# Kernel optimization log

Hardware: AMD Instinct MI355X
Metric: run time of the kernel (lower is better)

The kernel has to match this reference:

```python
import jax, jax.numpy as jnp
import numpy as np

NUM_LEVELS = 16
LEVEL_DIM = 2
BASE_RES = 16
LOG2_HASH = 24
DESIRED_RES = 2048
D = 2
PRIMES = (1, 2654435761)
N_POINTS = 2097152
HIDDEN = 64
OUT_DIM = 3
LC_INIT = 1e-4


def _level_meta():
    # torch-ngp gridencoder level geometry (align_corners=False)
    S = np.log2(DESIRED_RES / BASE_RES) / (NUM_LEVELS - 1)
    max_params = 2 ** LOG2_HASH
    scales, res, offsets = [], [], [0]
    for l in range(NUM_LEVELS):
        s = 2.0 ** (l * S) * BASE_RES - 1.0
        r = int(np.ceil(s)) + 1
        p = min(max_params, (r + 1) ** D)
        p = int(np.ceil(p / 8) * 8)  # align to 8
        scales.append(s)
        res.append(r)
        offsets.append(offsets[-1] + p)
    return scales, res, offsets

SCALES, RES, OFFSETS = _level_meta()
TOTAL_PARAMS = OFFSETS[-1]  # 8827256 for this config


def hashgrid_encode(x01, embeddings):
    # x01: [N, 2] in [0,1]; embeddings: [TOTAL_PARAMS, LEVEL_DIM]
    feats = []
    for l in range(NUM_LEVELS):
        scale, r = SCALES[l], RES[l]
        size = OFFSETS[l + 1] - OFFSETS[l]
        dense = (r + 1) ** D <= size  # all levels dense for 2D / log2=24
        pos = x01 * jnp.float32(scale) + 0.5
        pg = jnp.floor(pos)
        frac = pos - pg  # [N,2] bilinear weights
        pgi = pg.astype(jnp.uint32)
        acc = jnp.zeros((x01.shape[0], LEVEL_DIM), x01.dtype)
        for cx in (0, 1):
            for cy in (0, 1):
                gx = pgi[:, 0] + jnp.uint32(cx)
                gy = pgi[:, 1] + jnp.uint32(cy)
                if dense:
                    idx = gx + gy * jnp.uint32(r + 1)
                else:
                    idx = (gx * jnp.uint32(PRIMES[0])) ^ (gy * jnp.uint32(PRIMES[1]))
                idx = (idx % jnp.uint32(size)).astype(jnp.int32) + OFFSETS[l]
                wx = frac[:, 0] if cx else 1.0 - frac[:, 0]
                wy = frac[:, 1] if cy else 1.0 - frac[:, 1]
                acc = acc + (wx * wy)[:, None] * embeddings[idx]
        feats.append(acc)
    return jnp.concatenate(feats, axis=-1)  # [N, 32]


def setup_inputs():
    key = jax.random.key(0)
    ks = jax.random.split(key, 5)
    in_feat = NUM_LEVELS * LEVEL_DIM  # 32

    def lin(k, fan_in, fan_out):
        b = 1.0 / np.sqrt(fan_in)
        kw, kb = jax.random.split(k)
        w = jax.random.uniform(kw, (fan_out, fan_in), jnp.float32, -b, b)
        bb = jax.random.uniform(kb, (fan_out,), jnp.float32, -b, b)
        return w, bb

    w0, b0 = lin(ks[1], in_feat, HIDDEN)
    w1, b1 = lin(ks[2], HIDDEN, HIDDEN)
    w2, b2 = lin(ks[3], HIDDEN, OUT_DIM)
    return {
        "x": jax.random.uniform(ks[0], (N_POINTS, 2), jnp.float32),
        "cmax": jnp.ones((2,), jnp.float32),
        "embeddings": jax.random.uniform(ks[4], (TOTAL_PARAMS, LEVEL_DIM), jnp.float32, -LC_INIT, LC_INIT),
        "w0": w0, "b0": b0, "w1": w1, "b1": b1, "w2": w2, "b2": b2,
    }


def reference(x, cmax, embeddings, w0, b0, w1, b1, w2, b2):
    x01 = x / cmax[::-1][None]  # cmax.flip(-1)
    out_lc0 = hashgrid_encode(x01, embeddings)
    h = jax.nn.relu(out_lc0)            # lc_act='relu'
    h = jax.nn.relu(h @ w0.T + b0)      # layer 0
    h = jax.nn.relu(h @ w1.T + b1)      # layer 1
    h = h @ w2.T + b2                   # layer 2 (no act)
    return h, out_lc0
```

## Files before the change

### kernel.cpp

```cpp
#include <hip/hip_runtime.h>
#include <math.h>

#define NLEV 16
#define RES  256
#define NBIN 65536

typedef _Float16 f16;
typedef f16 f16x8 __attribute__((ext_vector_type(8)));
typedef float f32x4 __attribute__((ext_vector_type(4)));

struct LevelMeta {
    float scale[NLEV];
    int   r1[NLEV];
    int   off[NLEV];
};

struct alignas(8) F4 { float x, y, z, w; };

__device__ inline unsigned spread2d(unsigned v) {
    v = (v | (v << 4)) & 0x0F0Fu;
    v = (v | (v << 2)) & 0x3333u;
    v = (v | (v << 1)) & 0x5555u;
    return v;
}

__device__ inline unsigned bin_of(float x0, float x1) {
    int bx = (int)(x0 * (float)RES); bx = bx < 0 ? 0 : (bx > RES - 1 ? RES - 1 : bx);
    int by = (int)(x1 * (float)RES); by = by < 0 ? 0 : (by > RES - 1 ? RES - 1 : by);
    return spread2d((unsigned)bx) | (spread2d((unsigned)by) << 1);
}

__global__ __launch_bounds__(256)
void zero_kernel(unsigned* __restrict__ hist) {
    ((uint4*)hist)[blockIdx.x * 256 + threadIdx.x] = uint4{0, 0, 0, 0};
}

__global__ __launch_bounds__(256)
void hist_kernel(const float* __restrict__ x, const float* __restrict__ cmax,
                 unsigned* __restrict__ hist, unsigned* __restrict__ rec) {
    int p = blockIdx.x * 256 + threadIdx.x;
    float2 xy = ((const float2*)x)[p];
    unsigned b = bin_of(xy.x / cmax[1], xy.y / cmax[0]);
    unsigned s = atomicAdd(&hist[b], 1u);
    rec[p] = (b << 16) | (s & 0xFFFFu);
}

__global__ __launch_bounds__(256)
void scanA_kernel(const unsigned* __restrict__ hist, unsigned* __restrict__ sums) {
    __shared__ unsigned ws[4];
    int t = threadIdx.x;
    unsigned s = hist[blockIdx.x * 256 + t];
#pragma unroll
    for (int o = 1; o < 64; o <<= 1) s += (unsigned)__shfl_xor((int)s, o);
    if ((t & 63) == 0) ws[t >> 6] = s;
    __syncthreads();
    if (t == 0) sums[blockIdx.x] = ws[0] + ws[1] + ws[2] + ws[3];
}

__global__ __launch_bounds__(256)
void scanBC_kernel(const unsigned* __restrict__ hist, const unsigned* __restrict__ sums,
                   unsigned* __restrict__ base) {
    __shared__ unsigned ws[4];
    __shared__ unsigned chunk_base;
    int t = threadIdx.x, lane = t & 63, w = t >> 6;

    {
        unsigned v = (t < blockIdx.x) ? sums[t] : 0u;
#pragma unroll
        for (int o = 1; o < 64; o <<= 1) v += (unsigned)__shfl_xor((int)v, o);
        if (lane == 0) ws[w] = v;
        __syncthreads();
        if (t == 0) chunk_base = ws[0] + ws[1] + ws[2] + ws[3];
        __syncthreads();
    }

    int gb = blockIdx.x * 256 + t;
    unsigned v = hist[gb];
    unsigned xs = v;
#pragma unroll
    for (int o = 1; o < 64; o <<= 1) {
        unsigned y = (unsigned)__shfl_up((int)xs, o);
        if (lane >= o) xs += y;
    }
    __syncthreads();
    if (lane == 63) ws[w] = xs;
    __syncthreads();
    unsigned wo = 0;
    for (int k = 0; k < w; ++k) wo += ws[k];
    base[gb] = chunk_base + wo + xs - v;
}

__global__ __launch_bounds__(256)
void scatter_kernel(const float* __restrict__ x, const float* __restrict__ cmax,
                    const unsigned* __restrict__ rec,
                    const unsigned* __restrict__ base,
                    unsigned* __restrict__ pidx, float2* __restrict__ px) {
    int p = blockIdx.x * 256 + threadIdx.x;
    unsigned r = rec[p];
    unsigned rank = base[r >> 16] + (r & 0xFFFFu);
    pidx[rank] = (unsigned)p;
    float2 xy = ((const float2*)x)[p];
    float2 v; v.x = xy.x / cmax[1]; v.y = xy.y / cmax[0];
    px[rank] = v;
}

__global__ __launch_bounds__(256, 3)
void hashmlp_kernel(const float* __restrict__ x,
                    const float* __restrict__ cmax,
                    const unsigned* __restrict__ pidx,
                    const float2* __restrict__ px,
                    const float* __restrict__ emb,
                    const float* __restrict__ w0,
                    const float* __restrict__ b0,
                    const float* __restrict__ w1,
                    const float* __restrict__ b1,
                    const float* __restrict__ w2,
                    const float* __restrict__ b2,
                    float* __restrict__ out,
                    int npts, int nblk,
                    LevelMeta meta)
{
    __shared__ f16 w0s[64 * 40];
    __shared__ f16 w1s[64 * 72];
    __shared__ f16 w2s[16 * 72];
    __shared__ f16 wbuf[4][4608];

    const int tid  = threadIdx.x;
    const int lane = tid & 63;
    const int wave = tid >> 6;

    float w0t[8], w1t[16], w2t[4];
#pragma unroll
    for (int k = 0; k < 8; ++k)  w0t[k] = w0[tid + 256 * k];
#pragma unroll
    for (int k = 0; k < 16; ++k) w1t[k] = w1[tid + 256 * k];
#pragma unroll
    for (int k = 0; k < 4; ++k) {
        int i = tid + 256 * k; int r = i >> 6, c = i & 63;
        w2t[k] = (r < 3) ? w2[r * 64 + c] : 0.f;
    }

    int bid = blockIdx.x;
    int cpx = nblk >> 3;
    int swz = (bid & 7) * cpx + (bid >> 3);
    const int g = swz * 256 + tid;
    const int gblk = swz * 256 + wave * 64;

    int p;
    float x0, x1;
    if (pidx) {
        p = (int)pidx[g];
        float2 xy = px[g];
        x0 = xy.x; x1 = xy.y;
    } else {
        p = g;
        float2 xy = ((const float2*)x)[p];
        x0 = xy.x / cmax[1];
        x1 = xy.y / cmax[0];
    }

    float fr[32];
#pragma unroll
    for (int l = 0; l < NLEV; ++l) {
        const float sc = meta.scale[l];
        const int r1 = meta.r1[l];
        const int off = meta.off[l];
        float p0 = x0 * sc + 0.5f;
        float p1 = x1 * sc + 0.5f;
        float g0 = floorf(p0), g1 = floorf(p1);
        float f0 = p0 - g0, f1 = p1 - g1;
        int i0 = (int)g0, i1 = (int)g1;
        const float* ebf = emb + 2 * (off + i1 * r1 + i0);
        F4 lo = *(const F4*)ebf;
        F4 hi = *(const F4*)(ebf + 2 * r1);
        float omf0 = 1.f - f0, omf1 = 1.f - f1;
        float w00 = omf0 * omf1, w01 = omf0 * f1, w10 = f0 * omf1, w11 = f0 * f1;
        float a0 = w00 * lo.x; a0 += w01 * hi.x; a0 += w10 * lo.z; a0 += w11 * hi.z;
        float a1 = w00 * lo.y; a1 += w01 * hi.y; a1 += w10 * lo.w; a1 += w11 * hi.w;
        fr[2 * l]     = a0;
        fr[2 * l + 1] = a1;
    }

#pragma unroll
    for (int k = 0; k < 8; ++k)  { int i = tid + 256 * k; w0s[(i >> 5) * 40 + (i & 31)] = (f16)w0t[k]; }
#pragma unroll
    for (int k = 0; k < 16; ++k) { int i = tid + 256 * k; w1s[(i >> 6) * 72 + (i & 63)] = (f16)w1t[k]; }
#pragma unroll
    for (int k = 0; k < 4; ++k)  { int i = tid + 256 * k; w2s[(i >> 6) * 72 + (i & 63)] = (f16)w2t[k]; }

    float* outlc = out + (size_t)npts * 3 + (size_t)p * 32;
#pragma unroll
    for (int c = 0; c < 8; ++c) {
        float4 v;
        v.x = fr[4 * c]; v.y = fr[4 * c + 1]; v.z = fr[4 * c + 2]; v.w = fr[4 * c + 3];
        ((float4*)outlc)[c] = v;
    }

    f16* fbuf = wbuf[wave];
#pragma unroll
    for (int c = 0; c < 4; ++c) {
        f16x8 v;
#pragma unroll
        for (int j = 0; j < 8; ++j)
            v[j] = (f16)(fmaxf(fr[8 * c + j], 0.f) * 16384.f);
        *(f16x8*)&fbuf[lane * 40 + c * 8] = v;
    }

    __syncthreads();

    const int lr = lane & 15;
    const int lg = lane >> 4;
    f16* hbuf = wbuf[wave];

    {
        f16x8 bf[4];
        float bia[4];
#pragma unroll
        for (int nt = 0; nt < 4; ++nt) {
            bf[nt] = *(const f16x8*)&w0s[(nt * 16 + lr) * 40 + lg * 8];
            bia[nt] = b0[nt * 16 + lr];
        }
#pragma unroll
        for (int mt = 3; mt >= 0; --mt) {
            f16x8 a = *(const f16x8*)&fbuf[(mt * 16 + lr) * 40 + lg * 8];
#pragma unroll
            for (int nt = 0; nt < 4; ++nt) {
                f32x4 c = {0.f, 0.f, 0.f, 0.f};
                c = __builtin_amdgcn_mfma_f32_16x16x32_f16(a, bf[nt], c, 0, 0, 0);
#pragma unroll
                for (int q = 0; q < 4; ++q) {
                    float h = fmaxf(c[q] * (1.0f / 16384.f) + bia[nt], 0.f);
                    hbuf[(mt * 16 + lg * 4 + q) * 72 + nt * 16 + lr] = (f16)h;
                }
            }
        }
    }

    {
        f16x8 bf[4][2];
        float bia[4];
#pragma unroll
        for (int nt = 0; nt < 4; ++nt) {
            bf[nt][0] = *(const f16x8*)&w1s[(nt * 16 + lr) * 72 + lg * 8];
            bf[nt][1] = *(const f16x8*)&w1s[(nt * 16 + lr) * 72 + 32 + lg * 8];
            bia[nt] = b1[nt * 16 + lr];
        }
#pragma unroll
        for (int mt = 0; mt < 4; ++mt) {
            f16x8 a0 = *(const f16x8*)&hbuf[(mt * 16 + lr) * 72 + lg * 8];
            f16x8 a1 = *(const f16x8*)&hbuf[(mt * 16 + lr) * 72 + 32 + lg * 8];
#pragma unroll
            for (int nt = 0; nt < 4; ++nt) {
                f32x4 c = {0.f, 0.f, 0.f, 0.f};
                c = __builtin_amdgcn_mfma_f32_16x16x32_f16(a0, bf[nt][0], c, 0, 0, 0);
                c = __builtin_amdgcn_mfma_f32_16x16x32_f16(a1, bf[nt][1], c, 0, 0, 0);
#pragma unroll
                for (int q = 0; q < 4; ++q) {
                    float h = fmaxf(c[q] + bia[nt], 0.f);
                    hbuf[(mt * 16 + lg * 4 + q) * 72 + nt * 16 + lr] = (f16)h;
                }
            }
        }
    }

    {
        f16x8 bf0 = *(const f16x8*)&w2s[lr * 72 + lg * 8];
        f16x8 bf1 = *(const f16x8*)&w2s[lr * 72 + 32 + lg * 8];
        float bia2 = (lr < 3) ? b2[lr] : 0.f;
#pragma unroll
        for (int mt = 0; mt < 4; ++mt) {
            f16x8 a0 = *(const f16x8*)&hbuf[(mt * 16 + lr) * 72 + lg * 8];
            f16x8 a1 = *(const f16x8*)&hbuf[(mt * 16 + lr) * 72 + 32 + lg * 8];
            f32x4 c = {0.f, 0.f, 0.f, 0.f};
            c = __builtin_amdgcn_mfma_f32_16x16x32_f16(a0, bf0, c, 0, 0, 0);
            c = __builtin_amdgcn_mfma_f32_16x16x32_f16(a1, bf1, c, 0, 0, 0);
            if (lr < 3) {
#pragma unroll
                for (int q = 0; q < 4; ++q) {
                    int row = mt * 16 + lg * 4 + q;
                    int po = pidx ? (int)pidx[gblk + row] : (gblk + row);
                    out[(size_t)po * 3 + lr] = c[q] + bia2;
                }
            }
        }
    }
}

extern "C" void kernel_launch(void* const* d_in, const int* in_sizes, int n_in,
                              void* d_out, int out_size, void* d_ws, size_t ws_size,
                              hipStream_t stream) {
    const float* x    = (const float*)d_in[0];
    const float* cmax = (const float*)d_in[1];
    const float* emb  = (const float*)d_in[2];
    const float* w0   = (const float*)d_in[3];
    const float* b0   = (const float*)d_in[4];
    const float* w1   = (const float*)d_in[5];
    const float* b1   = (const float*)d_in[6];
    const float* w2   = (const float*)d_in[7];
    const float* b2   = (const float*)d_in[8];
    const int npts = in_sizes[0] / 2;
    const int nblk = npts / 256;

    LevelMeta meta;
    const double S = log2(2048.0 / 16.0) / 15.0;
    long long off = 0;
    for (int l = 0; l < NLEV; ++l) {
        double s = pow(2.0, l * S) * 16.0 - 1.0;
        int r = (int)ceil(s) + 1;
        long long pc = (long long)(r + 1) * (r + 1);
        if (pc > (1ll << 24)) pc = (1ll << 24);
        pc = ((pc + 7) / 8) * 8;
        meta.scale[l] = (float)s;
        meta.r1[l]    = r + 1;
        meta.off[l]   = (int)off;
        off += pc;
    }

    size_t need = (size_t)NBIN * 8 + 256 * 4 + (size_t)npts * 16;
    if (ws_size >= need && (npts & 255) == 0 && (nblk & 7) == 0) {
        unsigned* hist = (unsigned*)d_ws;
        unsigned* base = hist + NBIN;
        unsigned* sums = base + NBIN;
        unsigned* pidx = sums + 256;
        unsigned* rec  = pidx + npts;
        float2*   px   = (float2*)(rec + npts);

        hipLaunchKernelGGL(zero_kernel, dim3(NBIN / 1024), dim3(256), 0, stream, hist);
        hipLaunchKernelGGL(hist_kernel, dim3(nblk), dim3(256), 0, stream, x, cmax, hist, rec);
        hipLaunchKernelGGL(scanA_kernel, dim3(NBIN / 256), dim3(256), 0, stream, hist, sums);
        hipLaunchKernelGGL(scanBC_kernel, dim3(NBIN / 256), dim3(256), 0, stream, hist, sums, base);
        hipLaunchKernelGGL(scatter_kernel, dim3(nblk), dim3(256), 0, stream, x, cmax, rec, base, pidx, px);
        hipLaunchKernelGGL(hashmlp_kernel, dim3(nblk), dim3(256), 0, stream,
                           x, cmax, pidx, px, emb, w0, b0, w1, b1, w2, b2,
                           (float*)d_out, npts, nblk, meta);
    } else {
        hipLaunchKernelGGL(hashmlp_kernel, dim3(nblk), dim3(256), 0, stream,
                           x, cmax, (const unsigned*)nullptr, (const float2*)nullptr,
                           emb, w0, b0, w1, b1, w2, b2,
                           (float*)d_out, npts, nblk, meta);
    }
}
```

Before: 366.5 us.

## Process MLP in two 32-row halves per wave to raise occupancy to four blocks

The per-wave LDS staging buffer is halved. Each wave now runs the three MLP layers on 32 points at a time in two passes, with the weight fragments held in registers across both passes. This lets launch bounds ask for four blocks per CU instead of three, giving more waves to hide latency on the embedding gather. Weights are now written into LDS straight from global memory at kernel start instead of being held in registers across the gather. The cost is more live registers for the weight fragments under a tighter register budget, which risks spills, plus extra serialisation inside each wave.

```diff
diff --git a/kernel.cpp b/kernel.cpp
--- a/kernel.cpp
+++ b/kernel.cpp
@@ -104,7 +104,7 @@
     px[rank] = v;
 }
 
-__global__ __launch_bounds__(256, 3)
+__global__ __launch_bounds__(256, 4)
 void hashmlp_kernel(const float* __restrict__ x,
                     const float* __restrict__ cmax,
                     const unsigned* __restrict__ pidx,
@@ -123,21 +123,19 @@
     __shared__ f16 w0s[64 * 40];
     __shared__ f16 w1s[64 * 72];
     __shared__ f16 w2s[16 * 72];
-    __shared__ f16 wbuf[4][4608];
+    __shared__ f16 wbuf[4][2304];
 
     const int tid  = threadIdx.x;
     const int lane = tid & 63;
     const int wave = tid >> 6;
 
-    float w0t[8], w1t[16], w2t[4];
-#pragma unroll
-    for (int k = 0; k < 8; ++k)  w0t[k] = w0[tid + 256 * k];
-#pragma unroll
-    for (int k = 0; k < 16; ++k) w1t[k] = w1[tid + 256 * k];
-#pragma unroll
-    for (int k = 0; k < 4; ++k) {
-        int i = tid + 256 * k; int r = i >> 6, c = i & 63;
-        w2t[k] = (r < 3) ? w2[r * 64 + c] : 0.f;
+    for (int i = tid; i < 64 * 32; i += 256)
+        w0s[(i >> 5) * 40 + (i & 31)] = (f16)w0[i];
+    for (int i = tid; i < 64 * 64; i += 256)
+        w1s[(i >> 6) * 72 + (i & 63)] = (f16)w1[i];
+    for (int i = tid; i < 16 * 64; i += 256) {
+        int r = i >> 6, c = i & 63;
+        w2s[r * 72 + c] = (r < 3) ? (f16)w2[r * 64 + c] : (f16)0.f;
     }
 
     int bid = blockIdx.x;
@@ -181,13 +179,6 @@
         fr[2 * l + 1] = a1;
     }
 
-#pragma unroll
-    for (int k = 0; k < 8; ++k)  { int i = tid + 256 * k; w0s[(i >> 5) * 40 + (i & 31)] = (f16)w0t[k]; }
-#pragma unroll
-    for (int k = 0; k < 16; ++k) { int i = tid + 256 * k; w1s[(i >> 6) * 72 + (i & 63)] = (f16)w1t[k]; }
-#pragma unroll
-    for (int k = 0; k < 4; ++k)  { int i = tid + 256 * k; w2s[(i >> 6) * 72 + (i & 63)] = (f16)w2t[k]; }
-
     float* outlc = out + (size_t)npts * 3 + (size_t)p * 32;
 #pragma unroll
     for (int c = 0; c < 8; ++c) {
@@ -196,88 +187,87 @@
         ((float4*)outlc)[c] = v;
     }
 
-    f16* fbuf = wbuf[wave];
-#pragma unroll
-    for (int c = 0; c < 4; ++c) {
-        f16x8 v;
-#pragma unroll
-        for (int j = 0; j < 8; ++j)
-            v[j] = (f16)(fmaxf(fr[8 * c + j], 0.f) * 16384.f);
-        *(f16x8*)&fbuf[lane * 40 + c * 8] = v;
-    }
-
     __syncthreads();
 
     const int lr = lane & 15;
     const int lg = lane >> 4;
+    f16* fbuf = wbuf[wave];
     f16* hbuf = wbuf[wave];
 
-    {
-        f16x8 bf[4];
-        float bia[4];
-#pragma unroll
-        for (int nt = 0; nt < 4; ++nt) {
-            bf[nt] = *(const f16x8*)&w0s[(nt * 16 + lr) * 40 + lg * 8];
-            bia[nt] = b0[nt * 16 + lr];
+    f16x8 bf0l[4]; float bia0[4];
+#pragma unroll
+    for (int nt = 0; nt < 4; ++nt) {
+        bf0l[nt] = *(const f16x8*)&w0s[(nt * 16 + lr) * 40 + lg * 8];
+        bia0[nt] = b0[nt * 16 + lr];
+    }
+    f16x8 bf1l[4][2]; float bia1[4];
+#pragma unroll
+    for (int nt = 0; nt < 4; ++nt) {
+        bf1l[nt][0] = *(const f16x8*)&w1s[(nt * 16 + lr) * 72 + lg * 8];
+        bf1l[nt][1] = *(const f16x8*)&w1s[(nt * 16 + lr) * 72 + 32 + lg * 8];
+        bia1[nt] = b1[nt * 16 + lr];
+    }
+    f16x8 bf2a = *(const f16x8*)&w2s[lr * 72 + lg * 8];
+    f16x8 bf2b = *(const f16x8*)&w2s[lr * 72 + 32 + lg * 8];
+    float bia2 = (lr < 3) ? b2[lr] : 0.f;
+
+#pragma unroll
+    for (int hf = 0; hf < 2; ++hf) {
+        if ((lane >> 5) == hf) {
+            const int r = lane & 31;
+#pragma unroll
+            for (int c = 0; c < 4; ++c) {
+                f16x8 v;
+#pragma unroll
+                for (int j = 0; j < 8; ++j)
+                    v[j] = (f16)(fmaxf(fr[8 * c + j], 0.f) * 16384.f);
+                *(f16x8*)&fbuf[r * 40 + c * 8] = v;
+            }
         }
-#pragma unroll
-        for (int mt = 3; mt >= 0; --mt) {
-            f16x8 a = *(const f16x8*)&fbuf[(mt * 16 + lr) * 40 + lg * 8];
+
+#pragma unroll
+        for (int mtl = 1; mtl >= 0; --mtl) {
+            f16x8 a = *(const f16x8*)&fbuf[(mtl * 16 + lr) * 40 + lg * 8];
 #pragma unroll
             for (int nt = 0; nt < 4; ++nt) {
                 f32x4 c = {0.f, 0.f, 0.f, 0.f};
-                c = __builtin_amdgcn_mfma_f32_16x16x32_f16(a, bf[nt], c, 0, 0, 0);
+                c = __builtin_amdgcn_mfma_f32_16x16x32_f16(a, bf0l[nt], c, 0, 0, 0);
 #pragma unroll
                 for (int q = 0; q < 4; ++q) {
-                    float h = fmaxf(c[q] * (1.0f / 16384.f) + bia[nt], 0.f);
-                    hbuf[(mt * 16 + lg * 4 + q) * 72 + nt * 16 + lr] = (f16)h;
+                    float h = fmaxf(c[q] * (1.0f / 16384.f) + bia0[nt], 0.f);
+                    hbuf[(mtl * 16 + lg * 4 + q) * 72 + nt * 16 + lr] = (f16)h;
                 }
             }
         }
-    }
-
-    {
-        f16x8 bf[4][2];
-        float bia[4];
-#pragma unroll
-        for (int nt = 0; nt < 4; ++nt) {
-            bf[nt][0] = *(const f16x8*)&w1s[(nt * 16 + lr) * 72 + lg * 8];
-            bf[nt][1] = *(const f16x8*)&w1s[(nt * 16 + lr) * 72 + 32 + lg * 8];
-            bia[nt] = b1[nt * 16 + lr];
-        }
-#pragma unroll
-        for (int mt = 0; mt < 4; ++mt) {
-            f16x8 a0 = *(const f16x8*)&hbuf[(mt * 16 + lr) * 72 + lg * 8];
-            f16x8 a1 = *(const f16x8*)&hbuf[(mt * 16 + lr) * 72 + 32 + lg * 8];
+
+#pragma unroll
+        for (int mtl = 0; mtl < 2; ++mtl) {
+            f16x8 a0 = *(const f16x8*)&hbuf[(mtl * 16 + lr) * 72 + lg * 8];
+            f16x8 a1 = *(const f16x8*)&hbuf[(mtl * 16 + lr) * 72 + 32 + lg * 8];
 #pragma unroll
             for (int nt = 0; nt < 4; ++nt) {
                 f32x4 c = {0.f, 0.f, 0.f, 0.f};
-                c = __builtin_amdgcn_mfma_f32_16x16x32_f16(a0, bf[nt][0], c, 0, 0, 0);
-                c = __builtin_amdgcn_mfma_f32_16x16x32_f16(a1, bf[nt][1], c, 0, 0, 0);
+                c = __builtin_amdgcn_mfma_f32_16x16x32_f16(a0, bf1l[nt][0], c, 0, 0, 0);
+                c = __builtin_amdgcn_mfma_f32_16x16x32_f16(a1, bf1l[nt][1], c, 0, 0, 0);
 #pragma unroll
                 for (int q = 0; q < 4; ++q) {
-                    float h = fmaxf(c[q] + bia[nt], 0.f);
-                    hbuf[(mt * 16 + lg * 4 + q) * 72 + nt * 16 + lr] = (f16)h;
+                    float h = fmaxf(c[q] + bia1[nt], 0.f);
+                    hbuf[(mtl * 16 + lg * 4 + q) * 72 + nt * 16 + lr] = (f16)h;
                 }
             }
         }
-    }
-
-    {
-        f16x8 bf0 = *(const f16x8*)&w2s[lr * 72 + lg * 8];
-        f16x8 bf1 = *(const f16x8*)&w2s[lr * 72 + 32 + lg * 8];
-        float bia2 = (lr < 3) ? b2[lr] : 0.f;
-#pragma unroll
-        for (int mt = 0; mt < 4; ++mt) {
-            f16x8 a0 = *(const f16x8*)&hbuf[(mt * 16 + lr) * 72 + lg * 8];
-            f16x8 a1 = *(const f16x8*)&hbuf[(mt * 16 + lr) * 72 + 32 + lg * 8];
+
+#pragma unroll
+        for (int mtl = 0; mtl < 2; ++mtl) {
+            f16x8 a0 = *(const f16x8*)&hbuf[(mtl * 16 + lr) * 72 + lg * 8];
+            f16x8 a1 = *(const f16x8*)&hbuf[(mtl * 16 + lr) * 72 + 32 + lg * 8];
             f32x4 c = {0.f, 0.f, 0.f, 0.f};
-            c = __builtin_amdgcn_mfma_f32_16x16x32_f16(a0, bf0, c, 0, 0, 0);
-            c = __builtin_amdgcn_mfma_f32_16x16x32_f16(a1, bf1, c, 0, 0, 0);
+            c = __builtin_amdgcn_mfma_f32_16x16x32_f16(a0, bf2a, c, 0, 0, 0);
+            c = __builtin_amdgcn_mfma_f32_16x16x32_f16(a1, bf2b, c, 0, 0, 0);
             if (lr < 3) {
 #pragma unroll
                 for (int q = 0; q < 4; ++q) {
-                    int row = mt * 16 + lg * 4 + q;
+                    int row = hf * 32 + mtl * 16 + lg * 4 + q;
                     int po = pidx ? (int)pidx[gblk + row] : (gblk + row);
                     out[(size_t)po * 3 + lr] = c[q] + bia2;
                 }
```

Result: slower. 397.4 us (+8.4%).

## Replace global-atomic counting sort with block-local LDS histogram sort over coarser bins

Applied to the files above, without the earlier changes.

The spatial pre-sort moves from per-point global atomics into a 65536-bin histogram to a two-pass block-local scheme. 256 blocks each build a 4096-bin histogram in LDS, a per-bin scan across blocks and a single-block total scan follow, and a scatter pass recomputes ranks with LDS atomics. This removes global atomic contention, the rec buffer and one launch. Coarser 64x64 bins give a looser spatial locality order for the hash-grid gathers, and the scatter order within a bin is no longer deterministic.

```diff
diff --git a/kernel.cpp b/kernel.cpp
--- a/kernel.cpp
+++ b/kernel.cpp
@@ -2,8 +2,9 @@
 #include <math.h>
 
 #define NLEV 16
-#define RES  256
-#define NBIN 65536
+#define RES  64
+#define NBIN 4096
+#define SRTBLK 256
 
 typedef _Float16 f16;
 typedef f16 f16x8 __attribute__((ext_vector_type(8)));
@@ -30,78 +31,100 @@
     return spread2d((unsigned)bx) | (spread2d((unsigned)by) << 1);
 }
 
+__global__ __launch_bounds__(1024)
+void hist_kernel(const float* __restrict__ x, const float* __restrict__ cmax,
+                 unsigned* __restrict__ hist2d, int ppb) {
+    __shared__ unsigned lh[NBIN];
+    const int t = threadIdx.x, bid = blockIdx.x;
+    for (int i = t; i < NBIN; i += 1024) lh[i] = 0;
+    __syncthreads();
+    const float c0 = cmax[1], c1 = cmax[0];
+    const int base = bid * ppb;
+    for (int i = t; i < ppb; i += 1024) {
+        float2 xy = ((const float2*)x)[base + i];
+        atomicAdd(&lh[bin_of(xy.x / c0, xy.y / c1)], 1u);
+    }
+    __syncthreads();
+    for (int i = t; i < NBIN; i += 1024)
+        hist2d[i * SRTBLK + bid] = lh[i];
+}
+
 __global__ __launch_bounds__(256)
-void zero_kernel(unsigned* __restrict__ hist) {
-    ((uint4*)hist)[blockIdx.x * 256 + threadIdx.x] = uint4{0, 0, 0, 0};
-}
-
-__global__ __launch_bounds__(256)
-void hist_kernel(const float* __restrict__ x, const float* __restrict__ cmax,
-                 unsigned* __restrict__ hist, unsigned* __restrict__ rec) {
-    int p = blockIdx.x * 256 + threadIdx.x;
-    float2 xy = ((const float2*)x)[p];
-    unsigned b = bin_of(xy.x / cmax[1], xy.y / cmax[0]);
-    unsigned s = atomicAdd(&hist[b], 1u);
-    rec[p] = (b << 16) | (s & 0xFFFFu);
-}
-
-__global__ __launch_bounds__(256)
-void scanA_kernel(const unsigned* __restrict__ hist, unsigned* __restrict__ sums) {
-    __shared__ unsigned ws[4];
-    int t = threadIdx.x;
-    unsigned s = hist[blockIdx.x * 256 + t];
-#pragma unroll
-    for (int o = 1; o < 64; o <<= 1) s += (unsigned)__shfl_xor((int)s, o);
-    if ((t & 63) == 0) ws[t >> 6] = s;
-    __syncthreads();
-    if (t == 0) sums[blockIdx.x] = ws[0] + ws[1] + ws[2] + ws[3];
-}
-
-__global__ __launch_bounds__(256)
-void scanBC_kernel(const unsigned* __restrict__ hist, const unsigned* __restrict__ sums,
-                   unsigned* __restrict__ base) {
-    __shared__ unsigned ws[4];
-    __shared__ unsigned chunk_base;
-    int t = threadIdx.x, lane = t & 63, w = t >> 6;
-
-    {
-        unsigned v = (t < blockIdx.x) ? sums[t] : 0u;
-#pragma unroll
-        for (int o = 1; o < 64; o <<= 1) v += (unsigned)__shfl_xor((int)v, o);
-        if (lane == 0) ws[w] = v;
-        __syncthreads();
-        if (t == 0) chunk_base = ws[0] + ws[1] + ws[2] + ws[3];
-        __syncthreads();
-    }
-
-    int gb = blockIdx.x * 256 + t;
-    unsigned v = hist[gb];
-    unsigned xs = v;
+void scanbin_kernel(unsigned* __restrict__ hist2d, unsigned* __restrict__ binTot) {
+    const int wave = threadIdx.x >> 6, lane = threadIdx.x & 63;
+    const int bin = blockIdx.x * 4 + wave;
+    uint4* row = (uint4*)(hist2d + bin * SRTBLK);
+    uint4 v = row[lane];
+    unsigned s = v.x + v.y + v.z + v.w;
+    unsigned xs = s;
 #pragma unroll
     for (int o = 1; o < 64; o <<= 1) {
         unsigned y = (unsigned)__shfl_up((int)xs, o);
         if (lane >= o) xs += y;
     }
-    __syncthreads();
-    if (lane == 63) ws[w] = xs;
+    unsigned ex = xs - s;
+    uint4 w;
+    w.x = ex;
+    w.y = w.x + v.x;
+    w.z = w.y + v.y;
+    w.w = w.z + v.z;
+    row[lane] = w;
+    if (lane == 63) binTot[bin] = xs;
+}
+
+__global__ __launch_bounds__(256)
+void scantot_kernel(const unsigned* __restrict__ tot, unsigned* __restrict__ basev) {
+    __shared__ unsigned wsum[4];
+    int t = threadIdx.x;
+    unsigned v[16];
+    unsigned s = 0;
+#pragma unroll
+    for (int k = 0; k < 4; ++k) {
+        uint4 h = ((const uint4*)tot)[t * 4 + k];
+        v[4 * k] = h.x; v[4 * k + 1] = h.y; v[4 * k + 2] = h.z; v[4 * k + 3] = h.w;
+        s += h.x + h.y + h.z + h.w;
+    }
+    int lane = t & 63, w = t >> 6;
+    unsigned xs = s;
+#pragma unroll
+    for (int o = 1; o < 64; o <<= 1) {
+        unsigned y = (unsigned)__shfl_up((int)xs, o);
+        if (lane >= o) xs += y;
+    }
+    if (lane == 63) wsum[w] = xs;
     __syncthreads();
     unsigned wo = 0;
-    for (int k = 0; k < w; ++k) wo += ws[k];
-    base[gb] = chunk_base + wo + xs - v;
-}
-
-__global__ __launch_bounds__(256)
+    for (int k = 0; k < w; ++k) wo += wsum[k];
+    unsigned run = wo + xs - s;
+#pragma unroll
+    for (int j = 0; j < 16; ++j) {
+        basev[t * 16 + j] = run;
+        run += v[j];
+    }
+}
+
+__global__ __launch_bounds__(1024)
 void scatter_kernel(const float* __restrict__ x, const float* __restrict__ cmax,
-                    const unsigned* __restrict__ rec,
-                    const unsigned* __restrict__ base,
-                    unsigned* __restrict__ pidx, float2* __restrict__ px) {
-    int p = blockIdx.x * 256 + threadIdx.x;
-    unsigned r = rec[p];
-    unsigned rank = base[r >> 16] + (r & 0xFFFFu);
-    pidx[rank] = (unsigned)p;
-    float2 xy = ((const float2*)x)[p];
-    float2 v; v.x = xy.x / cmax[1]; v.y = xy.y / cmax[0];
-    px[rank] = v;
+                    const unsigned* __restrict__ pre2d,
+                    const unsigned* __restrict__ binBase,
+                    unsigned* __restrict__ pidx, float2* __restrict__ px, int ppb) {
+    __shared__ unsigned lseq[NBIN];
+    const int t = threadIdx.x, bid = blockIdx.x;
+    for (int i = t; i < NBIN; i += 1024) lseq[i] = 0;
+    __syncthreads();
+    const float c0 = cmax[1], c1 = cmax[0];
+    const int base = bid * ppb;
+    for (int i = t; i < ppb; i += 1024) {
+        int p = base + i;
+        float2 xy = ((const float2*)x)[p];
+        float x0 = xy.x / c0, x1 = xy.y / c1;
+        unsigned b = bin_of(x0, x1);
+        unsigned s = atomicAdd(&lseq[b], 1u);
+        unsigned rank = binBase[b] + pre2d[b * SRTBLK + bid] + s;
+        pidx[rank] = (unsigned)p;
+        float2 v; v.x = x0; v.y = x1;
+        px[rank] = v;
+    }
 }
 
 __global__ __launch_bounds__(256, 3)
@@ -316,20 +339,19 @@
         off += pc;
     }
 
-    size_t need = (size_t)NBIN * 8 + 256 * 4 + (size_t)npts * 16;
-    if (ws_size >= need && (npts & 255) == 0 && (nblk & 7) == 0) {
-        unsigned* hist = (unsigned*)d_ws;
-        unsigned* base = hist + NBIN;
-        unsigned* sums = base + NBIN;
-        unsigned* pidx = sums + 256;
-        unsigned* rec  = pidx + npts;
-        float2*   px   = (float2*)(rec + npts);
-
-        hipLaunchKernelGGL(zero_kernel, dim3(NBIN / 1024), dim3(256), 0, stream, hist);
-        hipLaunchKernelGGL(hist_kernel, dim3(nblk), dim3(256), 0, stream, x, cmax, hist, rec);
-        hipLaunchKernelGGL(scanA_kernel, dim3(NBIN / 256), dim3(256), 0, stream, hist, sums);
-        hipLaunchKernelGGL(scanBC_kernel, dim3(NBIN / 256), dim3(256), 0, stream, hist, sums, base);
-        hipLaunchKernelGGL(scatter_kernel, dim3(nblk), dim3(256), 0, stream, x, cmax, rec, base, pidx, px);
+    size_t need = (size_t)NBIN * SRTBLK * 4 + (size_t)NBIN * 8 + (size_t)npts * 12;
+    if (ws_size >= need && (npts % SRTBLK) == 0 && (npts & 255) == 0 && (nblk & 7) == 0) {
+        unsigned* hist2d  = (unsigned*)d_ws;
+        unsigned* binTot  = hist2d + (size_t)NBIN * SRTBLK;
+        unsigned* binBase = binTot + NBIN;
+        unsigned* pidx    = binBase + NBIN;
+        float2*   px      = (float2*)(pidx + npts);
+        const int ppb = npts / SRTBLK;
+
+        hipLaunchKernelGGL(hist_kernel, dim3(SRTBLK), dim3(1024), 0, stream, x, cmax, hist2d, ppb);
+        hipLaunchKernelGGL(scanbin_kernel, dim3(NBIN / 4), dim3(256), 0, stream, hist2d, binTot);
+        hipLaunchKernelGGL(scantot_kernel, dim3(1), dim3(256), 0, stream, binTot, binBase);
+        hipLaunchKernelGGL(scatter_kernel, dim3(SRTBLK), dim3(1024), 0, stream, x, cmax, hist2d, binBase, pidx, px, ppb);
         hipLaunchKernelGGL(hashmlp_kernel, dim3(nblk), dim3(256), 0, stream,
                            x, cmax, pidx, px, emb, w0, b0, w1, b1, w2, b2,
                            (float*)d_out, npts, nblk, meta);
```

New measurement: 324.7 us, median of 2. 1.13x faster.
